# Performance work log

Hardware: AMD Instinct MI355X
Metric: run time of the kernel (lower is better)

## Reference

```python
import jax, jax.numpy as jnp
import numpy as np

N = 20000          # nodes (== virtual nodes, forced by scatter dim_size + residuals)
E = 240000         # edges
H = 256            # hidden_dim
SD = 128           # scalar_dim (mult of 0e in "128x0e+64x1o+32x2e")
FEAT = 128 + 64 * 3 + 32 * 5   # 480 = target_irreps dim
C = 4              # vn_channel


def _lin(key, din, dout):
    k1, k2 = jax.random.split(key)
    s = 1.0 / np.sqrt(din)
    w = jax.random.uniform(k1, (din, dout), jnp.float32, -s, s)
    b = jax.random.uniform(k2, (dout,), jnp.float32, -s, s)
    return w, b


def _mlp(x, w1, b1, w2, b2):
    # BaseMLP: Linear -> SiLU -> Linear (no norm, no residual, no last act)
    return jax.nn.silu(x @ w1 + b1) @ w2 + b2


def setup_inputs() -> dict:
    key = jax.random.key(0)
    ks = jax.random.split(key, 12)
    inp = {
        "node_feat": jax.random.normal(ks[0], (N, FEAT), jnp.float32),
        "node_pos": jax.random.normal(ks[1], (N, 3), jnp.float32),
        "vn_feat": jax.random.normal(ks[2], (N, H), jnp.float32),
        "vn_pos": jax.random.normal(ks[3], (N, 3 * C), jnp.float32),
        "edge_index": jax.random.randint(ks[4], (2, E), 0, N),
        "w_scalar": jax.random.normal(ks[5], (SD, SD), jnp.float32),  # e3nn o3.Linear 0e->0e path
    }
    mlps = {"cm": (SD + H + C * C, H), "vr": (H, C), "rv": (H, C * C),
            "ft": (H, H), "f2t": (H, SD), "vf": (H, H)}
    i = 6
    for name, (din, dout) in mlps.items():
        k1, k2 = jax.random.split(ks[i]); i += 1
        inp[name + "_w1"], inp[name + "_b1"] = _lin(k1, din, H)
        inp[name + "_w2"], inp[name + "_b2"] = _lin(k2, H, dout)
    return inp


def reference(node_feat, node_pos, vn_feat, vn_pos, edge_index, w_scalar,
              cm_w1, cm_b1, cm_w2, cm_b2, vr_w1, vr_b1, vr_w2, vr_b2,
              rv_w1, rv_b1, rv_w2, rv_b2, ft_w1, ft_b1, ft_w2, ft_b2,
              f2t_w1, f2t_b1, f2t_w2, f2t_b2, vf_w1, vf_b1, vf_w2, vf_b2):
    n = node_feat.shape[0]
    row, col = edge_index[0], edge_index[1]

    # e3nn o3.Linear(target_irreps -> SDx0e): single 0e->0e path, 1/sqrt(fan_in)
    nfs = (node_feat[:, :SD] @ w_scalar) * (1.0 / np.sqrt(SD))

    # per-edge relative positions between node pos (tiled to C channels) and vn pos
    d = (jnp.tile(node_pos[row], (1, C)) - vn_pos[col]).reshape(-1, C, 3)  # [E,C,3]

    # normalized gram matrix of the C difference vectors
    ip = jnp.einsum('ecj,ekj->eck', d, d).reshape(-1, C * C)
    ip = ip / jnp.maximum(jnp.linalg.norm(ip, axis=-1, keepdims=True), 1e-8)

    dn = d / jnp.maximum(jnp.linalg.norm(d, axis=-1, keepdims=True), 1e-8)  # [E,C,3]

    msg = _mlp(jnp.concatenate([nfs[row], vn_feat[col], ip], axis=1),
               cm_w1, cm_b1, cm_w2, cm_b2)                                   # [E,H]

    w_vr = _mlp(msg, vr_w1, vr_b1, vr_w2, vr_b2)                 # [E,C]
    w_rv = _mlp(msg, rv_w1, rv_b1, rv_w2, rv_b2).reshape(-1, C, C)

    inv = 1.0 / np.sqrt(C)
    # FCTP Cx1o (x) 1x0e -> 1x1o  (x2 == 1): weighted sum of the C vectors
    vr_upd = inv * jnp.einsum('ec,ecj->ej', w_vr, dn)            # [E,3]
    # FCTP Cx1o (x) 1x0e -> Cx1o on -dn
    rv_upd = inv * jnp.einsum('ecu,ecj->euj', w_rv, -dn).reshape(-1, 3 * C)  # [E,3C]

    cnt = jnp.maximum(jax.ops.segment_sum(jnp.ones((row.shape[0],), msg.dtype), row, n), 1.0)[:, None]
    agg_feat = jax.ops.segment_sum(msg, row, n) / cnt            # scatter_mean by row
    agg_vr = jax.ops.segment_sum(vr_upd, row, n) / cnt
    agg_rv = jax.ops.segment_sum(rv_upd, row, n) / cnt

    ds = _mlp(_mlp(agg_feat, ft_w1, ft_b1, ft_w2, ft_b2), f2t_w1, f2t_b1, f2t_w2, f2t_b2)
    node_feat_out = node_feat.at[:, :SD].add(ds)  # delta only hits the scalar (0e) block
    node_pos_out = node_pos + agg_vr
    vn_feat_out = vn_feat + _mlp(agg_feat, vf_w1, vf_b1, vf_w2, vf_b2)
    vn_pos_out = vn_pos + agg_rv
    return node_feat_out, node_pos_out, vn_feat_out, vn_pos_out
```

## Files before the change

kernel.cpp:

```cpp
#include <hip/hip_runtime.h>
#include <hip/hip_bf16.h>
#include <math.h>


#define FEAT 480
#define HDIM 256
#define SDIM 128
#define MSTR 264

#define OW1   0
#define OW2   106496
#define OVR1  172032
#define ORV1  237568
#define OVR2  303104
#define ORV2  307200
#define OFT1  311296
#define OFT2  376832
#define OF2T1 442368
#define OF2T2 507904
#define OVF1  540672
#define OVF2  606208
#define OWTOT 671744

typedef __attribute__((ext_vector_type(8))) short bf16x8;
typedef __attribute__((ext_vector_type(4))) float f32x4;

__device__ __forceinline__ float rcp_f(float x) {
    return __builtin_amdgcn_rcpf(x);
}
__device__ __forceinline__ float silu_f(float x) {
    return x * rcp_f(1.0f + __expf(-x));
}
__device__ __forceinline__ ushort f2b(float v) {
    __hip_bfloat16 h = __float2bfloat16(v);
    return *(ushort*)&h;
}
__device__ __forceinline__ float b2f(ushort u) {
    union { unsigned int i; float f; } c;
    c.i = ((unsigned int)u) << 16;
    return c.f;
}

#define KLOOP2(SRC, WP)                                                        \
    {                                                                          \
        _Pragma("unroll")                                                      \
        for (int mt = 0; mt < 4; ++mt)                                         \
            _Pragma("unroll")                                                  \
            for (int nt = 0; nt < 2; ++nt) acc[mt][nt] = (f32x4)0.f;           \
        _Pragma("unroll")                                                      \
        for (int ks = 0; ks < 8; ++ks) {                                       \
            bf16x8 a_[4];                                                      \
            _Pragma("unroll")                                                  \
            for (int mt = 0; mt < 4; ++mt)                                     \
                a_[mt] = *(const bf16x8*)&(SRC)[(mt * 16 + lr) * MSTR + ks * 32 + lk * 8]; \
            _Pragma("unroll")                                                  \
            for (int nt = 0; nt < 2; ++nt) {                                   \
                const bf16x8 b = *(const bf16x8*)&(WP)[(size_t)(((wv * 2 + nt) * 8 + ks) * 512) + lane * 8]; \
                _Pragma("unroll")                                              \
                for (int mt = 0; mt < 4; ++mt)                                 \
                    acc[mt][nt] = __builtin_amdgcn_mfma_f32_16x16x32_bf16(a_[mt], b, acc[mt][nt], 0, 0, 0); \
            }                                                                  \
        }                                                                      \
    }

#define EPI_SILU2(DST, BIAS)                                                   \
    _Pragma("unroll")                                                          \
    for (int nt = 0; nt < 2; ++nt) {                                           \
        const int col = colBase + nt * 16 + lr;                                \
        const float bb = (BIAS)[col];                                          \
        _Pragma("unroll")                                                      \
        for (int mt = 0; mt < 4; ++mt)                                         \
            _Pragma("unroll")                                                  \
            for (int r = 0; r < 4; ++r) {                                      \
                const int row = mt * 16 + lk * 4 + r;                          \
                (DST)[row * MSTR + col] = f2b(silu_f(acc[mt][nt][r] + bb));    \
            }                                                                  \
    }

#define KLOOP_FR(SRC, WP)                                                      \
    {                                                                          \
        _Pragma("unroll")                                                      \
        for (int mt = 0; mt < 2; ++mt)                                         \
            _Pragma("unroll")                                                  \
            for (int nt = 0; nt < 4; ++nt) accn[mt][nt] = (f32x4)0.f;          \
        _Pragma("unroll")                                                      \
        for (int ks = 0; ks < 8; ++ks) {                                       \
            const bf16x8 a0 = *(const bf16x8*)&(SRC)[lr * MSTR + ks * 32 + lk * 8];        \
            const bf16x8 a1 = *(const bf16x8*)&(SRC)[(lr + 16) * MSTR + ks * 32 + lk * 8]; \
            _Pragma("unroll")                                                  \
            for (int nt = 0; nt < 4; ++nt) {                                   \
                const bf16x8 b = *(const bf16x8*)&(WP)[(size_t)(((wv * 4 + nt) * 8 + ks) * 512) + lane * 8]; \
                accn[0][nt] = __builtin_amdgcn_mfma_f32_16x16x32_bf16(a0, b, accn[0][nt], 0, 0, 0); \
                accn[1][nt] = __builtin_amdgcn_mfma_f32_16x16x32_bf16(a1, b, accn[1][nt], 0, 0, 0); \
            }                                                                  \
        }                                                                      \
    }

#define EPI_SILUN(DST, BIAS)                                                   \
    _Pragma("unroll")                                                          \
    for (int nt = 0; nt < 4; ++nt) {                                           \
        const int col = colBase + nt * 16 + lr;                                \
        const float bb = (BIAS)[col];                                          \
        _Pragma("unroll")                                                      \
        for (int mt = 0; mt < 2; ++mt)                                         \
            _Pragma("unroll")                                                  \
            for (int r = 0; r < 4; ++r) {                                      \
                const int row = mt * 16 + lk * 4 + r;                          \
                (DST)[row * MSTR + col] = f2b(silu_f(accn[mt][nt][r] + bb));   \
            }                                                                  \
    }

__global__ __launch_bounds__(256) void k_count(
    const int* __restrict__ eidx, int* __restrict__ cnt_i, int E)
{
    const int e = blockIdx.x * 256 + threadIdx.x;
    if (e < E) atomicAdd(&cnt_i[eidx[e]], 1);
}

__global__ __launch_bounds__(1024) void k_scanA(
    const int* __restrict__ cnt_i, int* __restrict__ rowstart,
    float* __restrict__ cntf, int* __restrict__ bsum, int Nn)
{
    __shared__ int sh[1024];
    const int t = threadIdx.x;
    const int i = blockIdx.x * 1024 + t;
    const int v = (i < Nn) ? cnt_i[i] : 0;
    sh[t] = v;
    __syncthreads();
    for (int off = 1; off < 1024; off <<= 1) {
        const int add = (t >= off) ? sh[t - off] : 0;
        __syncthreads();
        sh[t] += add;
        __syncthreads();
    }
    if (i < Nn) {
        rowstart[i + 1] = sh[t];
        cntf[i] = fmaxf((float)v, 1.0f);
    }
    if (t == 1023) bsum[blockIdx.x] = sh[t];
}

__global__ __launch_bounds__(64) void k_scanB(int* __restrict__ bsum, int nb)
{
    if (threadIdx.x == 0) {
        int s = 0;
        for (int i = 0; i < nb; ++i) { const int v = bsum[i]; bsum[i] = s; s += v; }
    }
}

__global__ __launch_bounds__(1024) void k_scanC(
    int* __restrict__ rowstart, const int* __restrict__ bsum, int Nn)
{
    const int i = blockIdx.x * 1024 + threadIdx.x;
    if (i < Nn) rowstart[i + 1] += bsum[blockIdx.x];
    if (i == 0) rowstart[0] = 0;
}

__global__ __launch_bounds__(256) void k_place(
    const int* __restrict__ eidx, const int* __restrict__ rowstart,
    int* __restrict__ cursor, int* __restrict__ elist, int E)
{
    const int e = blockIdx.x * 256 + threadIdx.x;
    if (e < E) {
        const int r = eidx[e];
        const int p = atomicAdd(&cursor[r], 1);
        elist[rowstart[r] + p] = e;
    }
}

__global__ __launch_bounds__(256) void k_wprep(
    const float* __restrict__ w1, const float* __restrict__ w2,
    const float* __restrict__ vrw1, const float* __restrict__ rvw1,
    const float* __restrict__ vrw2, const float* __restrict__ rvw2,
    const float* __restrict__ ftw1, const float* __restrict__ ftw2,
    const float* __restrict__ f2tw1, const float* __restrict__ f2tw2,
    const float* __restrict__ vfw1, const float* __restrict__ vfw2,
    ushort* __restrict__ wb)
{
    const int idx = blockIdx.x * 256 + threadIdx.x;
    if (idx >= OWTOT) return;
    ushort v;
    if (idx < OW2) {
        const int o = idx, f = o >> 9, l = (o >> 3) & 63, e = o & 7;
        const int nt = f / 13, ks = f % 13;
        const int col = nt * 16 + (l & 15);
        const int k = ks * 32 + ((l >> 4) << 3) + e;
        v = (k < 400) ? f2b(w1[(size_t)k * 256 + col]) : (ushort)0;
    } else if (idx < OVR1) {
        const int o = idx - OW2, f = o >> 9, l = (o >> 3) & 63, e = o & 7;
        const int col = (f >> 3) * 16 + (l & 15);
        const int k = (f & 7) * 32 + ((l >> 4) << 3) + e;
        v = f2b(w2[(size_t)k * 256 + col]);
    } else if (idx < ORV1) {
        const int o = idx - OVR1, f = o >> 9, l = (o >> 3) & 63, e = o & 7;
        const int col = (f >> 3) * 16 + (l & 15);
        const int k = (f & 7) * 32 + ((l >> 4) << 3) + e;
        v = f2b(vrw1[(size_t)k * 256 + col]);
    } else if (idx < OVR2) {
        const int o = idx - ORV1, f = o >> 9, l = (o >> 3) & 63, e = o & 7;
        const int col = (f >> 3) * 16 + (l & 15);
        const int k = (f & 7) * 32 + ((l >> 4) << 3) + e;
        v = f2b(rvw1[(size_t)k * 256 + col]);
    } else if (idx < ORV2) {
        const int o = idx - OVR2, f = o >> 9, l = (o >> 3) & 63, e = o & 7;
        const int col = l & 15;
        const int k = f * 32 + ((l >> 4) << 3) + e;
        v = (col < 4) ? f2b(vrw2[(size_t)k * 4 + col]) : (ushort)0;
    } else if (idx < OFT1) {
        const int o = idx - ORV2, f = o >> 9, l = (o >> 3) & 63, e = o & 7;
        const int col = l & 15;
        const int k = f * 32 + ((l >> 4) << 3) + e;
        v = f2b(rvw2[(size_t)k * 16 + col]);
    } else if (idx < OFT2) {
        const int o = idx - OFT1, f = o >> 9, l = (o >> 3) & 63, e = o & 7;
        const int col = (f >> 3) * 16 + (l & 15);
        const int k = (f & 7) * 32 + ((l >> 4) << 3) + e;
        v = f2b(ftw1[(size_t)k * 256 + col]);
    } else if (idx < OF2T1) {
        const int o = idx - OFT2, f = o >> 9, l = (o >> 3) & 63, e = o & 7;
        const int col = (f >> 3) * 16 + (l & 15);
        const int k = (f & 7) * 32 + ((l >> 4) << 3) + e;
        v = f2b(ftw2[(size_t)k * 256 + col]);
    } else if (idx < OF2T2) {
        const int o = idx - OF2T1, f = o >> 9, l = (o >> 3) & 63, e = o & 7;
        const int col = (f >> 3) * 16 + (l & 15);
        const int k = (f & 7) * 32 + ((l >> 4) << 3) + e;
        v = f2b(f2tw1[(size_t)k * 256 + col]);
    } else if (idx < OVF1) {
        const int o = idx - OF2T2, f = o >> 9, l = (o >> 3) & 63, e = o & 7;
        const int col = (f >> 3) * 16 + (l & 15);
        const int k = (f & 7) * 32 + ((l >> 4) << 3) + e;
        v = f2b(f2tw2[(size_t)k * 128 + col]);
    } else if (idx < OVF2) {
        const int o = idx - OVF1, f = o >> 9, l = (o >> 3) & 63, e = o & 7;
        const int col = (f >> 3) * 16 + (l & 15);
        const int k = (f & 7) * 32 + ((l >> 4) << 3) + e;
        v = f2b(vfw1[(size_t)k * 256 + col]);
    } else {
        const int o = idx - OVF2, f = o >> 9, l = (o >> 3) & 63, e = o & 7;
        const int col = (f >> 3) * 16 + (l & 15);
        const int k = (f & 7) * 32 + ((l >> 4) << 3) + e;
        v = f2b(vfw2[(size_t)k * 256 + col]);
    }
    wb[idx] = v;
}

__global__ __launch_bounds__(256) void k_vnb(
    const float* __restrict__ vn_feat, ushort* __restrict__ vnb, int total4)
{
    const int i = blockIdx.x * 256 + threadIdx.x;
    if (i >= total4) return;
    const float4 v = *(const float4*)&vn_feat[(size_t)i * 4];
    ushort4 o;
    o.x = f2b(v.x); o.y = f2b(v.y); o.z = f2b(v.z); o.w = f2b(v.w);
    *(ushort4*)&vnb[(size_t)i * 4] = o;
}

__global__ __launch_bounds__(256) void k_nfs(
    const float* __restrict__ node_feat, const float* __restrict__ w_scalar,
    ushort* __restrict__ nfsb)
{
    __shared__ float At[32][20];
    __shared__ float Wt[16][128];
    const int t  = threadIdx.x;
    const int m0 = blockIdx.x * 32;
    const int c4 = (t & 31) * 4;
    const int rg = t >> 5;
    float acc[4][4] = {};
    for (int k0 = 0; k0 < 128; k0 += 16) {
        if (t < 128) {
            const int r = t >> 2, kk = (t & 3) * 4;
            *(float4*)&At[r][kk] =
                *(const float4*)&node_feat[(size_t)(m0 + r) * FEAT + k0 + kk];
        }
        #pragma unroll
        for (int i = 0; i < 2; ++i) {
            const int p  = t + i * 256;
            const int wr = p >> 5, wc = (p & 31) * 4;
            *(float4*)&Wt[wr][wc] =
                *(const float4*)&w_scalar[(size_t)(k0 + wr) * SDIM + wc];
        }
        __syncthreads();
        #pragma unroll
        for (int kk = 0; kk < 16; ++kk) {
            const float4 w = *(const float4*)&Wt[kk][c4];
            #pragma unroll
            for (int j = 0; j < 4; ++j) {
                const float a = At[rg * 4 + j][kk];
                acc[j][0] = fmaf(a, w.x, acc[j][0]);
                acc[j][1] = fmaf(a, w.y, acc[j][1]);
                acc[j][2] = fmaf(a, w.z, acc[j][2]);
                acc[j][3] = fmaf(a, w.w, acc[j][3]);
            }
        }
        __syncthreads();
    }
    const float s = 0.08838834764831845f;
    #pragma unroll
    for (int j = 0; j < 4; ++j) {
        ushort4 o;
        o.x = f2b(acc[j][0] * s); o.y = f2b(acc[j][1] * s);
        o.z = f2b(acc[j][2] * s); o.w = f2b(acc[j][3] * s);
        *(ushort4*)&nfsb[(size_t)(m0 + rg * 4 + j) * SDIM + c4] = o;
    }
}

__global__ __launch_bounds__(512, 4) void k_edge(
    const ushort* __restrict__ nfsb, const ushort* __restrict__ vnb,
    const float* __restrict__ node_pos, const float* __restrict__ vn_pos,
    const int* __restrict__ eidx, const int* __restrict__ elist,
    const ushort* __restrict__ wb,
    const float* __restrict__ b1, const float* __restrict__ b2,
    const float* __restrict__ vrb1, const float* __restrict__ vrb2,
    const float* __restrict__ rvb1, const float* __restrict__ rvb2,
    float* __restrict__ agg_feat, float* __restrict__ agg_vr,
    float* __restrict__ agg_rv, int E)
{
    __shared__ ushort Mg[64 * MSTR];
    __shared__ ushort Hd[64 * MSTR];
    __shared__ ushort ipB[64 * 16];
    __shared__ float dnS[64][12];
    __shared__ float wvrS[64][4];
    __shared__ float wrvS[64][16];
    __shared__ int rowi[64], coli[64];

    const int t  = threadIdx.x;
    const int e0 = blockIdx.x * 64;
    const int wv = t >> 6;
    const int lane = t & 63;
    const int lr = lane & 15;
    const int lk = lane >> 4;
    const int colBase = wv * 32;

    if (t < 64) {
        const int e = elist[e0 + t];
        const int r = eidx[e];
        const int c = eidx[E + e];
        rowi[t] = r; coli[t] = c;
        const float px = node_pos[r * 3 + 0];
        const float py = node_pos[r * 3 + 1];
        const float pz = node_pos[r * 3 + 2];
        float d[4][3];
        #pragma unroll
        for (int ch = 0; ch < 4; ++ch) {
            d[ch][0] = px - vn_pos[(size_t)c * 12 + ch * 3 + 0];
            d[ch][1] = py - vn_pos[(size_t)c * 12 + ch * 3 + 1];
            d[ch][2] = pz - vn_pos[(size_t)c * 12 + ch * 3 + 2];
        }
        float ss = 0.f, ipv[16];
        #pragma unroll
        for (int ci = 0; ci < 4; ++ci)
            #pragma unroll
            for (int ck = 0; ck < 4; ++ck) {
                const float v = d[ci][0]*d[ck][0] + d[ci][1]*d[ck][1] + d[ci][2]*d[ck][2];
                ipv[ci * 4 + ck] = v; ss += v * v;
            }
        const float inrm = rcp_f(fmaxf(sqrtf(ss), 1e-8f));
        #pragma unroll
        for (int i = 0; i < 16; ++i) ipB[t * 16 + i] = f2b(ipv[i] * inrm);
        #pragma unroll
        for (int ch = 0; ch < 4; ++ch) {
            const float nn = sqrtf(d[ch][0]*d[ch][0] + d[ch][1]*d[ch][1] + d[ch][2]*d[ch][2]);
            const float s = rcp_f(fmaxf(nn, 1e-8f));
            dnS[t][ch * 3 + 0] = d[ch][0] * s;
            dnS[t][ch * 3 + 1] = d[ch][1] * s;
            dnS[t][ch * 3 + 2] = d[ch][2] * s;
        }
    }
    __syncthreads();

    const ushort* nA[4]; const ushort* vA[4];
    #pragma unroll
    for (int mt = 0; mt < 4; ++mt) {
        nA[mt] = nfsb + (size_t)rowi[mt * 16 + lr] * SDIM + lk * 8;
        vA[mt] = vnb  + (size_t)coli[mt * 16 + lr] * HDIM + lk * 8;
    }
    const ushort* w1t = wb + OW1;

    f32x4 acc[4][2];

    #pragma unroll
    for (int mt = 0; mt < 4; ++mt)
        #pragma unroll
        for (int nt = 0; nt < 2; ++nt) acc[mt][nt] = (f32x4)0.f;
    #pragma unroll
    for (int ks = 0; ks < 13; ++ks) {
        bf16x8 a_[4];
        #pragma unroll
        for (int mt = 0; mt < 4; ++mt) {
            if (ks < 4)       a_[mt] = *(const bf16x8*)(nA[mt] + ks * 32);
            else if (ks < 12) a_[mt] = *(const bf16x8*)(vA[mt] + ks * 32 - 128);
            else if (lk < 2)  a_[mt] = *(const bf16x8*)&ipB[(mt * 16 + lr) * 16 + lk * 8];
            else              a_[mt] = (bf16x8)(short)0;
        }
        #pragma unroll
        for (int nt = 0; nt < 2; ++nt) {
            const bf16x8 b = *(const bf16x8*)&w1t[(size_t)(((wv * 2 + nt) * 13 + ks) * 512) + lane * 8];
            #pragma unroll
            for (int mt = 0; mt < 4; ++mt)
                acc[mt][nt] = __builtin_amdgcn_mfma_f32_16x16x32_bf16(a_[mt], b, acc[mt][nt], 0, 0, 0);
        }
    }
    EPI_SILU2(Hd, b1);
    __syncthreads();

    KLOOP2(Hd, wb + OW2);
    #pragma unroll
    for (int nt = 0; nt < 2; ++nt) {
        const int col = colBase + nt * 16 + lr;
        const float bb = b2[col];
        #pragma unroll
        for (int mt = 0; mt < 4; ++mt)
            #pragma unroll
            for (int r = 0; r < 4; ++r) {
                const int row = mt * 16 + lk * 4 + r;
                Mg[row * MSTR + col] = f2b(acc[mt][nt][r] + bb);
            }
    }
    __syncthreads();

    {
        const int col = t & 255;
        const int r0 = (t >> 8) * 32;
        float s = 0.f;
        int prev = rowi[r0];
        for (int r = r0; r < r0 + 32; ++r) {
            const int rr = rowi[r];
            if (rr != prev) {
                atomicAdd(&agg_feat[(size_t)prev * HDIM + col], s);
                s = 0.f; prev = rr;
            }
            s += b2f(Mg[r * MSTR + col]);
        }
        atomicAdd(&agg_feat[(size_t)prev * HDIM + col], s);
    }

    KLOOP2(Mg, wb + OVR1);
    EPI_SILU2(Hd, vrb1);

    KLOOP2(Mg, wb + ORV1);
    __syncthreads();
    #pragma unroll
    for (int nt = 0; nt < 2; ++nt) {
        const int col = colBase + nt * 16 + lr;
        const float br = rvb1[col];
        #pragma unroll
        for (int mt = 0; mt < 4; ++mt)
            #pragma unroll
            for (int r = 0; r < 4; ++r) {
                const int row = mt * 16 + lk * 4 + r;
                Mg[row * MSTR + col] = f2b(silu_f(acc[mt][nt][r] + br));
            }
    }
    __syncthreads();

    if ((wv & 3) == 0) {
        const int rb = (wv >> 2) * 32;
        const ushort* vrw2t = wb + OVR2;
        f32x4 a2[2]; a2[0] = (f32x4)0.f; a2[1] = (f32x4)0.f;
        #pragma unroll
        for (int ks = 0; ks < 8; ++ks) {
            const bf16x8 a0 = *(const bf16x8*)&Hd[(rb + lr) * MSTR + ks * 32 + lk * 8];
            const bf16x8 a1 = *(const bf16x8*)&Hd[(rb + 16 + lr) * MSTR + ks * 32 + lk * 8];
            const bf16x8 b  = *(const bf16x8*)&vrw2t[(size_t)(ks * 512) + lane * 8];
            a2[0] = __builtin_amdgcn_mfma_f32_16x16x32_bf16(a0, b, a2[0], 0, 0, 0);
            a2[1] = __builtin_amdgcn_mfma_f32_16x16x32_bf16(a1, b, a2[1], 0, 0, 0);
        }
        if (lr < 4) {
            const float bb = vrb2[lr];
            #pragma unroll
            for (int mt = 0; mt < 2; ++mt)
                #pragma unroll
                for (int r = 0; r < 4; ++r)
                    wvrS[rb + mt * 16 + lk * 4 + r][lr] = a2[mt][r] + bb;
        }
    } else if ((wv & 3) == 1) {
        const int rb = (wv >> 2) * 32;
        const ushort* rvw2t = wb + ORV2;
        f32x4 a2[2]; a2[0] = (f32x4)0.f; a2[1] = (f32x4)0.f;
        #pragma unroll
        for (int ks = 0; ks < 8; ++ks) {
            const bf16x8 a0 = *(const bf16x8*)&Mg[(rb + lr) * MSTR + ks * 32 + lk * 8];
            const bf16x8 a1 = *(const bf16x8*)&Mg[(rb + 16 + lr) * MSTR + ks * 32 + lk * 8];
            const bf16x8 b  = *(const bf16x8*)&rvw2t[(size_t)(ks * 512) + lane * 8];
            a2[0] = __builtin_amdgcn_mfma_f32_16x16x32_bf16(a0, b, a2[0], 0, 0, 0);
            a2[1] = __builtin_amdgcn_mfma_f32_16x16x32_bf16(a1, b, a2[1], 0, 0, 0);
        }
        const float bb = rvb2[lr];
        #pragma unroll
        for (int mt = 0; mt < 2; ++mt)
            #pragma unroll
            for (int r = 0; r < 4; ++r)
                wrvS[rb + mt * 16 + lk * 4 + r][lr] = a2[mt][r] + bb;
    }
    __syncthreads();

    if (t < 64) {
        float wvv[4], wrr[16], dn[12], ev[15];
        #pragma unroll
        for (int c = 0; c < 4; ++c)  wvv[c] = wvrS[t][c];
        #pragma unroll
        for (int i = 0; i < 16; ++i) wrr[i] = wrvS[t][i];
        #pragma unroll
        for (int i = 0; i < 12; ++i) dn[i]  = dnS[t][i];
        #pragma unroll
        for (int j = 0; j < 3; ++j) {
            float v = 0.f;
            #pragma unroll
            for (int c = 0; c < 4; ++c) v = fmaf(wvv[c], dn[c * 3 + j], v);
            ev[j] = 0.5f * v;
        }
        #pragma unroll
        for (int u = 0; u < 4; ++u)
            #pragma unroll
            for (int j = 0; j < 3; ++j) {
                float v = 0.f;
                #pragma unroll
                for (int c = 0; c < 4; ++c) v = fmaf(wrr[c * 4 + u], dn[c * 3 + j], v);
                ev[3 + u * 3 + j] = -0.5f * v;
            }
        #pragma unroll
        for (int i = 0; i < 15; ++i) wrvS[t][i] = ev[i];
    }
    __syncthreads();

    if ((t & 255) < 15) {
        const int comp = t & 255;
        const int r0 = (t >> 8) * 32;
        float s = 0.f;
        int prev = rowi[r0];
        for (int r = r0; r < r0 + 32; ++r) {
            const int rr = rowi[r];
            if (rr != prev) {
                if (comp < 3) atomicAdd(&agg_vr[(size_t)prev * 3 + comp], s);
                else          atomicAdd(&agg_rv[(size_t)prev * 12 + (comp - 3)], s);
                s = 0.f; prev = rr;
            }
            s += wrvS[r][comp];
        }
        if (comp < 3) atomicAdd(&agg_vr[(size_t)prev * 3 + comp], s);
        else          atomicAdd(&agg_rv[(size_t)prev * 12 + (comp - 3)], s);
    }
}

__global__ __launch_bounds__(256, 4) void k_node(
    const float* __restrict__ node_feat, const float* __restrict__ node_pos,
    const float* __restrict__ vn_feat, const float* __restrict__ vn_pos,
    const float* __restrict__ agg_feat, const float* __restrict__ agg_vr,
    const float* __restrict__ agg_rv, const float* __restrict__ cntf,
    const ushort* __restrict__ wb,
    const float* __restrict__ ftb1, const float* __restrict__ ftb2,
    const float* __restrict__ f2tb1, const float* __restrict__ f2tb2,
    const float* __restrict__ vfb1, const float* __restrict__ vfb2,
    float* __restrict__ out, int Nn)
{
    __shared__ ushort Ab[32 * MSTR];
    __shared__ ushort Hd[32 * MSTR];
    __shared__ float rc[32];
    const int t  = threadIdx.x;
    const int n0 = blockIdx.x * 32;
    const int wv = t >> 6;
    const int lane = t & 63;
    const int lr = lane & 15;
    const int lk = lane >> 4;
    const int colBase = wv * 64;

    float* nf_out = out;
    float* np_out = out + (size_t)Nn * FEAT;
    float* vf_out = np_out + (size_t)Nn * 3;
    float* vp_out = vf_out + (size_t)Nn * HDIM;

    if (t < 32) rc[t] = rcp_f(fmaxf(cntf[n0 + t], 1.0f));
    __syncthreads();
    #pragma unroll
    for (int i = 0; i < 8; ++i) {
        const int p = t + i * 256;
        const int r = p >> 6, cc = (p & 63) * 4;
        float4 v = *(const float4*)&agg_feat[(size_t)(n0 + r) * HDIM + cc];
        const float s = rc[r];
        ushort4 o;
        o.x = f2b(v.x * s); o.y = f2b(v.y * s);
        o.z = f2b(v.z * s); o.w = f2b(v.w * s);
        *(ushort4*)&Ab[r * MSTR + cc] = o;
    }
    __syncthreads();

    f32x4 accn[2][4];

    KLOOP_FR(Ab, wb + OVF1);
    EPI_SILUN(Hd, vfb1);
    __syncthreads();
    KLOOP_FR(Hd, wb + OVF2);
    #pragma unroll
    for (int nt = 0; nt < 4; ++nt) {
        const int col = colBase + nt * 16 + lr;
        const float bb = vfb2[col];
        #pragma unroll
        for (int mt = 0; mt < 2; ++mt)
            #pragma unroll
            for (int r = 0; r < 4; ++r) {
                const int row = mt * 16 + lk * 4 + r;
                const size_t o = (size_t)(n0 + row) * HDIM + col;
                vf_out[o] = vn_feat[o] + accn[mt][nt][r] + bb;
            }
    }
    __syncthreads();

    KLOOP_FR(Ab, wb + OFT1);
    EPI_SILUN(Hd, ftb1);
    __syncthreads();
    KLOOP_FR(Hd, wb + OFT2);
    #pragma unroll
    for (int nt = 0; nt < 4; ++nt) {
        const int col = colBase + nt * 16 + lr;
        const float bb = ftb2[col];
        #pragma unroll
        for (int mt = 0; mt < 2; ++mt)
            #pragma unroll
            for (int r = 0; r < 4; ++r) {
                const int row = mt * 16 + lk * 4 + r;
                Ab[row * MSTR + col] = f2b(accn[mt][nt][r] + bb);
            }
    }
    __syncthreads();

    KLOOP_FR(Ab, wb + OF2T1);
    EPI_SILUN(Hd, f2tb1);
    __syncthreads();
    {
        const ushort* w2p = wb + OF2T2;
        f32x4 a2[2][2];
        #pragma unroll
        for (int mt = 0; mt < 2; ++mt)
            #pragma unroll
            for (int nt = 0; nt < 2; ++nt) a2[mt][nt] = (f32x4)0.f;
        #pragma unroll
        for (int ks = 0; ks < 8; ++ks) {
            const int k0 = ks * 32 + lk * 8;
            const bf16x8 a0 = *(const bf16x8*)&Hd[lr * MSTR + k0];
            const bf16x8 a1 = *(const bf16x8*)&Hd[(lr + 16) * MSTR + k0];
            const bf16x8 w0 = *(const bf16x8*)&w2p[(size_t)(((wv * 2 + 0) * 8 + ks) * 512) + lane * 8];
            const bf16x8 w1v = *(const bf16x8*)&w2p[(size_t)(((wv * 2 + 1) * 8 + ks) * 512) + lane * 8];
            a2[0][0] = __builtin_amdgcn_mfma_f32_16x16x32_bf16(a0, w0, a2[0][0], 0, 0, 0);
            a2[1][0] = __builtin_amdgcn_mfma_f32_16x16x32_bf16(a1, w0, a2[1][0], 0, 0, 0);
            a2[0][1] = __builtin_amdgcn_mfma_f32_16x16x32_bf16(a0, w1v, a2[0][1], 0, 0, 0);
            a2[1][1] = __builtin_amdgcn_mfma_f32_16x16x32_bf16(a1, w1v, a2[1][1], 0, 0, 0);
        }
        #pragma unroll
        for (int nt = 0; nt < 2; ++nt) {
            const int col = wv * 32 + nt * 16 + lr;
            const float bb = f2tb2[col];
            #pragma unroll
            for (int mt = 0; mt < 2; ++mt)
                #pragma unroll
                for (int r = 0; r < 4; ++r) {
                    const int row = mt * 16 + lk * 4 + r;
                    const size_t o = (size_t)(n0 + row) * FEAT + col;
                    nf_out[o] = node_feat[o] + a2[mt][nt][r] + bb;
                }
        }
    }

    for (int p = t; p < 32 * 88; p += 256) {
        const int r = p / 88;
        const int cc = 128 + (p % 88) * 4;
        const size_t o = (size_t)(n0 + r) * FEAT + cc;
        *(float4*)&nf_out[o] = *(const float4*)&node_feat[o];
    }
    if (t < 32) {
        const int n = n0 + t;
        const float s = rc[t];
        #pragma unroll
        for (int j = 0; j < 3; ++j)
            np_out[(size_t)n * 3 + j] = node_pos[(size_t)n * 3 + j] + agg_vr[(size_t)n * 3 + j] * s;
        #pragma unroll
        for (int j = 0; j < 12; ++j)
            vp_out[(size_t)n * 12 + j] = vn_pos[(size_t)n * 12 + j] + agg_rv[(size_t)n * 12 + j] * s;
    }
}

extern "C" void kernel_launch(void* const* d_in, const int* in_sizes, int n_in,
                              void* d_out, int out_size, void* d_ws, size_t ws_size,
                              hipStream_t stream)
{
    (void)n_in; (void)out_size; (void)ws_size;
    const float* node_feat = (const float*)d_in[0];
    const float* node_pos  = (const float*)d_in[1];
    const float* vn_feat   = (const float*)d_in[2];
    const float* vn_pos    = (const float*)d_in[3];
    const int*   eidx      = (const int*)d_in[4];
    const float* w_scalar  = (const float*)d_in[5];
    const float* cm_w1  = (const float*)d_in[6];
    const float* cm_b1  = (const float*)d_in[7];
    const float* cm_w2  = (const float*)d_in[8];
    const float* cm_b2  = (const float*)d_in[9];
    const float* vr_w1  = (const float*)d_in[10];
    const float* vr_b1  = (const float*)d_in[11];
    const float* vr_w2  = (const float*)d_in[12];
    const float* vr_b2  = (const float*)d_in[13];
    const float* rv_w1  = (const float*)d_in[14];
    const float* rv_b1  = (const float*)d_in[15];
    const float* rv_w2  = (const float*)d_in[16];
    const float* rv_b2  = (const float*)d_in[17];
    const float* ft_w1  = (const float*)d_in[18];
    const float* ft_b1  = (const float*)d_in[19];
    const float* ft_w2  = (const float*)d_in[20];
    const float* ft_b2  = (const float*)d_in[21];
    const float* f2t_w1 = (const float*)d_in[22];
    const float* f2t_b1 = (const float*)d_in[23];
    const float* f2t_w2 = (const float*)d_in[24];
    const float* f2t_b2 = (const float*)d_in[25];
    const float* vf_w1  = (const float*)d_in[26];
    const float* vf_b1  = (const float*)d_in[27];
    const float* vf_w2  = (const float*)d_in[28];
    const float* vf_b2  = (const float*)d_in[29];

    const int Nn = in_sizes[0] / FEAT;
    const int E  = in_sizes[4] / 2;

    float* ws       = (float*)d_ws;
    float* agg_feat = ws;
    float* agg_vr   = agg_feat + (size_t)Nn * HDIM;
    float* agg_rv   = agg_vr   + (size_t)Nn * 3;
    float* cntf     = agg_rv   + (size_t)Nn * 12;
    int*   cnt_i    = (int*)(cntf + Nn);
    int*   cursor   = cnt_i + Nn;
    int*   rowstart = cursor + Nn;
    int*   bsum     = rowstart + Nn + 8;
    int*   elist    = bsum + 64;
    ushort* nfsb = (ushort*)(elist + E);
    ushort* vnb  = nfsb + (size_t)Nn * SDIM;
    ushort* wb   = vnb  + (size_t)Nn * HDIM;

    const size_t zero_bytes = (size_t)Nn * (HDIM + 3 + 12 + 1 + 2) * sizeof(float);
    hipMemsetAsync(agg_feat, 0, zero_bytes, stream);

    const int eg = (E + 255) / 256;
    const int sb = (Nn + 1023) / 1024;
    k_count<<<eg, 256, 0, stream>>>(eidx, cnt_i, E);
    k_scanA<<<sb, 1024, 0, stream>>>(cnt_i, rowstart, cntf, bsum, Nn);
    k_scanB<<<1, 64, 0, stream>>>(bsum, sb);
    k_scanC<<<sb, 1024, 0, stream>>>(rowstart, bsum, Nn);
    k_place<<<eg, 256, 0, stream>>>(eidx, rowstart, cursor, elist, E);
    k_wprep<<<(OWTOT + 255) / 256, 256, 0, stream>>>(
        cm_w1, cm_w2, vr_w1, rv_w1, vr_w2, rv_w2,
        ft_w1, ft_w2, f2t_w1, f2t_w2, vf_w1, vf_w2, wb);
    k_vnb<<<(Nn * 64 + 255) / 256, 256, 0, stream>>>(vn_feat, vnb, Nn * 64);
    k_nfs<<<Nn / 32, 256, 0, stream>>>(node_feat, w_scalar, nfsb);
    k_edge<<<E / 64, 512, 0, stream>>>(nfsb, vnb, node_pos, vn_pos, eidx, elist,
                                       wb, cm_b1, cm_b2, vr_b1, vr_b2, rv_b1, rv_b2,
                                       agg_feat, agg_vr, agg_rv, E);
    k_node<<<Nn / 32, 256, 0, stream>>>(node_feat, node_pos, vn_feat, vn_pos,
                                        agg_feat, agg_vr, agg_rv, cntf, wb,
                                        ft_b1, ft_b2, f2t_b1, f2t_b2, vf_b1, vf_b2,
                                        (float*)d_out, Nn);
}
```

Before: 431.8 us.

## Merge preprocessing kernels into one launch and fold block-sum scan into scanC

```diff
diff --git a/kernel.cpp b/kernel.cpp
--- a/kernel.cpp
+++ b/kernel.cpp
@@ -21,6 +21,10 @@
 #define OVF1  540672
 #define OVF2  606208
 #define OWTOT 671744
+
+#define NB_WPREP 2624
+#define NB_VNB   5000
+#define NB_NFS   625
 
 typedef __attribute__((ext_vector_type(8))) short bf16x8;
 typedef __attribute__((ext_vector_type(4))) float f32x4;
@@ -110,11 +114,141 @@
             }                                                                  \
     }
 
-__global__ __launch_bounds__(256) void k_count(
+__global__ __launch_bounds__(256) void k_prep(
+    const float* __restrict__ w1, const float* __restrict__ w2,
+    const float* __restrict__ vrw1, const float* __restrict__ rvw1,
+    const float* __restrict__ vrw2, const float* __restrict__ rvw2,
+    const float* __restrict__ ftw1, const float* __restrict__ ftw2,
+    const float* __restrict__ f2tw1, const float* __restrict__ f2tw2,
+    const float* __restrict__ vfw1, const float* __restrict__ vfw2,
+    ushort* __restrict__ wb,
+    const float* __restrict__ vn_feat, ushort* __restrict__ vnb,
+    const float* __restrict__ node_feat, const float* __restrict__ w_scalar,
+    ushort* __restrict__ nfsb,
     const int* __restrict__ eidx, int* __restrict__ cnt_i, int E)
 {
-    const int e = blockIdx.x * 256 + threadIdx.x;
-    if (e < E) atomicAdd(&cnt_i[eidx[e]], 1);
+    __shared__ float At[32][20];
+    __shared__ float Wt[16][128];
+    const int bid = blockIdx.x;
+    const int t = threadIdx.x;
+
+    if (bid < NB_WPREP) {
+        const int idx = bid * 256 + t;
+        ushort v;
+        if (idx < OW2) {
+            const int o = idx, f = o >> 9, l = (o >> 3) & 63, e = o & 7;
+            const int nt = f / 13, ks = f % 13;
+            const int col = nt * 16 + (l & 15);
+            const int k = ks * 32 + ((l >> 4) << 3) + e;
+            v = (k < 400) ? f2b(w1[(size_t)k * 256 + col]) : (ushort)0;
+        } else if (idx < OVR1) {
+            const int o = idx - OW2, f = o >> 9, l = (o >> 3) & 63, e = o & 7;
+            const int col = (f >> 3) * 16 + (l & 15);
+            const int k = (f & 7) * 32 + ((l >> 4) << 3) + e;
+            v = f2b(w2[(size_t)k * 256 + col]);
+        } else if (idx < ORV1) {
+            const int o = idx - OVR1, f = o >> 9, l = (o >> 3) & 63, e = o & 7;
+            const int col = (f >> 3) * 16 + (l & 15);
+            const int k = (f & 7) * 32 + ((l >> 4) << 3) + e;
+            v = f2b(vrw1[(size_t)k * 256 + col]);
+        } else if (idx < OVR2) {
+            const int o = idx - ORV1, f = o >> 9, l = (o >> 3) & 63, e = o & 7;
+            const int col = (f >> 3) * 16 + (l & 15);
+            const int k = (f & 7) * 32 + ((l >> 4) << 3) + e;
+            v = f2b(rvw1[(size_t)k * 256 + col]);
+        } else if (idx < ORV2) {
+            const int o = idx - OVR2, f = o >> 9, l = (o >> 3) & 63, e = o & 7;
+            const int col = l & 15;
+            const int k = f * 32 + ((l >> 4) << 3) + e;
+            v = (col < 4) ? f2b(vrw2[(size_t)k * 4 + col]) : (ushort)0;
+        } else if (idx < OFT1) {
+            const int o = idx - ORV2, f = o >> 9, l = (o >> 3) & 63, e = o & 7;
+            const int col = l & 15;
+            const int k = f * 32 + ((l >> 4) << 3) + e;
+            v = f2b(rvw2[(size_t)k * 16 + col]);
+        } else if (idx < OFT2) {
+            const int o = idx - OFT1, f = o >> 9, l = (o >> 3) & 63, e = o & 7;
+            const int col = (f >> 3) * 16 + (l & 15);
+            const int k = (f & 7) * 32 + ((l >> 4) << 3) + e;
+            v = f2b(ftw1[(size_t)k * 256 + col]);
+        } else if (idx < OF2T1) {
+            const int o = idx - OFT2, f = o >> 9, l = (o >> 3) & 63, e = o & 7;
+            const int col = (f >> 3) * 16 + (l & 15);
+            const int k = (f & 7) * 32 + ((l >> 4) << 3) + e;
+            v = f2b(ftw2[(size_t)k * 256 + col]);
+        } else if (idx < OF2T2) {
+            const int o = idx - OF2T1, f = o >> 9, l = (o >> 3) & 63, e = o & 7;
+            const int col = (f >> 3) * 16 + (l & 15);
+            const int k = (f & 7) * 32 + ((l >> 4) << 3) + e;
+            v = f2b(f2tw1[(size_t)k * 256 + col]);
+        } else if (idx < OVF1) {
+            const int o = idx - OF2T2, f = o >> 9, l = (o >> 3) & 63, e = o & 7;
+            const int col = (f >> 3) * 16 + (l & 15);
+            const int k = (f & 7) * 32 + ((l >> 4) << 3) + e;
+            v = f2b(f2tw2[(size_t)k * 128 + col]);
+        } else if (idx < OVF2) {
+            const int o = idx - OVF1, f = o >> 9, l = (o >> 3) & 63, e = o & 7;
+            const int col = (f >> 3) * 16 + (l & 15);
+            const int k = (f & 7) * 32 + ((l >> 4) << 3) + e;
+            v = f2b(vfw1[(size_t)k * 256 + col]);
+        } else {
+            const int o = idx - OVF2, f = o >> 9, l = (o >> 3) & 63, e = o & 7;
+            const int col = (f >> 3) * 16 + (l & 15);
+            const int k = (f & 7) * 32 + ((l >> 4) << 3) + e;
+            v = f2b(vfw2[(size_t)k * 256 + col]);
+        }
+        wb[idx] = v;
+    } else if (bid < NB_WPREP + NB_VNB) {
+        const int i = (bid - NB_WPREP) * 256 + t;
+        const float4 v = *(const float4*)&vn_feat[(size_t)i * 4];
+        ushort4 o;
+        o.x = f2b(v.x); o.y = f2b(v.y); o.z = f2b(v.z); o.w = f2b(v.w);
+        *(ushort4*)&vnb[(size_t)i * 4] = o;
+    } else if (bid < NB_WPREP + NB_VNB + NB_NFS) {
+        const int m0 = (bid - NB_WPREP - NB_VNB) * 32;
+        const int c4 = (t & 31) * 4;
+        const int rg = t >> 5;
+        float acc[4][4] = {};
+        for (int k0 = 0; k0 < 128; k0 += 16) {
+            if (t < 128) {
+                const int r = t >> 2, kk = (t & 3) * 4;
+                *(float4*)&At[r][kk] =
+                    *(const float4*)&node_feat[(size_t)(m0 + r) * FEAT + k0 + kk];
+            }
+            #pragma unroll
+            for (int i = 0; i < 2; ++i) {
+                const int p  = t + i * 256;
+                const int wr = p >> 5, wc = (p & 31) * 4;
+                *(float4*)&Wt[wr][wc] =
+                    *(const float4*)&w_scalar[(size_t)(k0 + wr) * SDIM + wc];
+            }
+            __syncthreads();
+            #pragma unroll
+            for (int kk = 0; kk < 16; ++kk) {
+                const float4 w = *(const float4*)&Wt[kk][c4];
+                #pragma unroll
+                for (int j = 0; j < 4; ++j) {
+                    const float a = At[rg * 4 + j][kk];
+                    acc[j][0] = fmaf(a, w.x, acc[j][0]);
+                    acc[j][1] = fmaf(a, w.y, acc[j][1]);
+                    acc[j][2] = fmaf(a, w.z, acc[j][2]);
+                    acc[j][3] = fmaf(a, w.w, acc[j][3]);
+                }
+            }
+            __syncthreads();
+        }
+        const float s = 0.08838834764831845f;
+        #pragma unroll
+        for (int j = 0; j < 4; ++j) {
+            ushort4 o;
+            o.x = f2b(acc[j][0] * s); o.y = f2b(acc[j][1] * s);
+            o.z = f2b(acc[j][2] * s); o.w = f2b(acc[j][3] * s);
+            *(ushort4*)&nfsb[(size_t)(m0 + rg * 4 + j) * SDIM + c4] = o;
+        }
+    } else {
+        const int e = (bid - NB_WPREP - NB_VNB - NB_NFS) * 256 + t;
+        if (e < E) atomicAdd(&cnt_i[eidx[e]], 1);
+    }
 }
 
 __global__ __launch_bounds__(1024) void k_scanA(
@@ -140,19 +274,19 @@
     if (t == 1023) bsum[blockIdx.x] = sh[t];
 }
 
-__global__ __launch_bounds__(64) void k_scanB(int* __restrict__ bsum, int nb)
-{
-    if (threadIdx.x == 0) {
-        int s = 0;
-        for (int i = 0; i < nb; ++i) { const int v = bsum[i]; bsum[i] = s; s += v; }
-    }
-}
-
 __global__ __launch_bounds__(1024) void k_scanC(
     int* __restrict__ rowstart, const int* __restrict__ bsum, int Nn)
 {
-    const int i = blockIdx.x * 1024 + threadIdx.x;
-    if (i < Nn) rowstart[i + 1] += bsum[blockIdx.x];
+    __shared__ int carry_s;
+    const int t = threadIdx.x;
+    if (t == 0) {
+        int s = 0;
+        for (int b = 0; b < (int)blockIdx.x; ++b) s += bsum[b];
+        carry_s = s;
+    }
+    __syncthreads();
+    const int i = blockIdx.x * 1024 + t;
+    if (i < Nn) rowstart[i + 1] += carry_s;
     if (i == 0) rowstart[0] = 0;
 }
 
@@ -165,143 +299,6 @@
         const int r = eidx[e];
         const int p = atomicAdd(&cursor[r], 1);
         elist[rowstart[r] + p] = e;
-    }
-}
-
-__global__ __launch_bounds__(256) void k_wprep(
-    const float* __restrict__ w1, const float* __restrict__ w2,
-    const float* __restrict__ vrw1, const float* __restrict__ rvw1,
-    const float* __restrict__ vrw2, const float* __restrict__ rvw2,
-    const float* __restrict__ ftw1, const float* __restrict__ ftw2,
-    const float* __restrict__ f2tw1, const float* __restrict__ f2tw2,
-    const float* __restrict__ vfw1, const float* __restrict__ vfw2,
-    ushort* __restrict__ wb)
-{
-    const int idx = blockIdx.x * 256 + threadIdx.x;
-    if (idx >= OWTOT) return;
-    ushort v;
-    if (idx < OW2) {
-        const int o = idx, f = o >> 9, l = (o >> 3) & 63, e = o & 7;
-        const int nt = f / 13, ks = f % 13;
-        const int col = nt * 16 + (l & 15);
-        const int k = ks * 32 + ((l >> 4) << 3) + e;
-        v = (k < 400) ? f2b(w1[(size_t)k * 256 + col]) : (ushort)0;
-    } else if (idx < OVR1) {
-        const int o = idx - OW2, f = o >> 9, l = (o >> 3) & 63, e = o & 7;
-        const int col = (f >> 3) * 16 + (l & 15);
-        const int k = (f & 7) * 32 + ((l >> 4) << 3) + e;
-        v = f2b(w2[(size_t)k * 256 + col]);
-    } else if (idx < ORV1) {
-        const int o = idx - OVR1, f = o >> 9, l = (o >> 3) & 63, e = o & 7;
-        const int col = (f >> 3) * 16 + (l & 15);
-        const int k = (f & 7) * 32 + ((l >> 4) << 3) + e;
-        v = f2b(vrw1[(size_t)k * 256 + col]);
-    } else if (idx < OVR2) {
-        const int o = idx - ORV1, f = o >> 9, l = (o >> 3) & 63, e = o & 7;
-        const int col = (f >> 3) * 16 + (l & 15);
-        const int k = (f & 7) * 32 + ((l >> 4) << 3) + e;
-        v = f2b(rvw1[(size_t)k * 256 + col]);
-    } else if (idx < ORV2) {
-        const int o = idx - OVR2, f = o >> 9, l = (o >> 3) & 63, e = o & 7;
-        const int col = l & 15;
-        const int k = f * 32 + ((l >> 4) << 3) + e;
-        v = (col < 4) ? f2b(vrw2[(size_t)k * 4 + col]) : (ushort)0;
-    } else if (idx < OFT1) {
-        const int o = idx - ORV2, f = o >> 9, l = (o >> 3) & 63, e = o & 7;
-        const int col = l & 15;
-        const int k = f * 32 + ((l >> 4) << 3) + e;
-        v = f2b(rvw2[(size_t)k * 16 + col]);
-    } else if (idx < OFT2) {
-        const int o = idx - OFT1, f = o >> 9, l = (o >> 3) & 63, e = o & 7;
-        const int col = (f >> 3) * 16 + (l & 15);
-        const int k = (f & 7) * 32 + ((l >> 4) << 3) + e;
-        v = f2b(ftw1[(size_t)k * 256 + col]);
-    } else if (idx < OF2T1) {
-        const int o = idx - OFT2, f = o >> 9, l = (o >> 3) & 63, e = o & 7;
-        const int col = (f >> 3) * 16 + (l & 15);
-        const int k = (f & 7) * 32 + ((l >> 4) << 3) + e;
-        v = f2b(ftw2[(size_t)k * 256 + col]);
-    } else if (idx < OF2T2) {
-        const int o = idx - OF2T1, f = o >> 9, l = (o >> 3) & 63, e = o & 7;
-        const int col = (f >> 3) * 16 + (l & 15);
-        const int k = (f & 7) * 32 + ((l >> 4) << 3) + e;
-        v = f2b(f2tw1[(size_t)k * 256 + col]);
-    } else if (idx < OVF1) {
-        const int o = idx - OF2T2, f = o >> 9, l = (o >> 3) & 63, e = o & 7;
-        const int col = (f >> 3) * 16 + (l & 15);
-        const int k = (f & 7) * 32 + ((l >> 4) << 3) + e;
-        v = f2b(f2tw2[(size_t)k * 128 + col]);
-    } else if (idx < OVF2) {
-        const int o = idx - OVF1, f = o >> 9, l = (o >> 3) & 63, e = o & 7;
-        const int col = (f >> 3) * 16 + (l & 15);
-        const int k = (f & 7) * 32 + ((l >> 4) << 3) + e;
-        v = f2b(vfw1[(size_t)k * 256 + col]);
-    } else {
-        const int o = idx - OVF2, f = o >> 9, l = (o >> 3) & 63, e = o & 7;
-        const int col = (f >> 3) * 16 + (l & 15);
-        const int k = (f & 7) * 32 + ((l >> 4) << 3) + e;
-        v = f2b(vfw2[(size_t)k * 256 + col]);
-    }
-    wb[idx] = v;
-}
-
-__global__ __launch_bounds__(256) void k_vnb(
-    const float* __restrict__ vn_feat, ushort* __restrict__ vnb, int total4)
-{
-    const int i = blockIdx.x * 256 + threadIdx.x;
-    if (i >= total4) return;
-    const float4 v = *(const float4*)&vn_feat[(size_t)i * 4];
-    ushort4 o;
-    o.x = f2b(v.x); o.y = f2b(v.y); o.z = f2b(v.z); o.w = f2b(v.w);
-    *(ushort4*)&vnb[(size_t)i * 4] = o;
-}
-
-__global__ __launch_bounds__(256) void k_nfs(
-    const float* __restrict__ node_feat, const float* __restrict__ w_scalar,
-    ushort* __restrict__ nfsb)
-{
-    __shared__ float At[32][20];
-    __shared__ float Wt[16][128];
-    const int t  = threadIdx.x;
-    const int m0 = blockIdx.x * 32;
-    const int c4 = (t & 31) * 4;
-    const int rg = t >> 5;
-    float acc[4][4] = {};
-    for (int k0 = 0; k0 < 128; k0 += 16) {
-        if (t < 128) {
-            const int r = t >> 2, kk = (t & 3) * 4;
-            *(float4*)&At[r][kk] =
-                *(const float4*)&node_feat[(size_t)(m0 + r) * FEAT + k0 + kk];
-        }
-        #pragma unroll
-        for (int i = 0; i < 2; ++i) {
-            const int p  = t + i * 256;
-            const int wr = p >> 5, wc = (p & 31) * 4;
-            *(float4*)&Wt[wr][wc] =
-                *(const float4*)&w_scalar[(size_t)(k0 + wr) * SDIM + wc];
-        }
-        __syncthreads();
-        #pragma unroll
-        for (int kk = 0; kk < 16; ++kk) {
-            const float4 w = *(const float4*)&Wt[kk][c4];
-            #pragma unroll
-            for (int j = 0; j < 4; ++j) {
-                const float a = At[rg * 4 + j][kk];
-                acc[j][0] = fmaf(a, w.x, acc[j][0]);
-                acc[j][1] = fmaf(a, w.y, acc[j][1]);
-                acc[j][2] = fmaf(a, w.z, acc[j][2]);
-                acc[j][3] = fmaf(a, w.w, acc[j][3]);
-            }
-        }
-        __syncthreads();
-    }
-    const float s = 0.08838834764831845f;
-    #pragma unroll
-    for (int j = 0; j < 4; ++j) {
-        ushort4 o;
-        o.x = f2b(acc[j][0] * s); o.y = f2b(acc[j][1] * s);
-        o.z = f2b(acc[j][2] * s); o.w = f2b(acc[j][3] * s);
-        *(ushort4*)&nfsb[(size_t)(m0 + rg * 4 + j) * SDIM + c4] = o;
     }
 }
 
@@ -737,16 +734,14 @@
 
     const int eg = (E + 255) / 256;
     const int sb = (Nn + 1023) / 1024;
-    k_count<<<eg, 256, 0, stream>>>(eidx, cnt_i, E);
+    k_prep<<<NB_WPREP + NB_VNB + NB_NFS + eg, 256, 0, stream>>>(
+        cm_w1, cm_w2, vr_w1, rv_w1, vr_w2, rv_w2,
+        ft_w1, ft_w2, f2t_w1, f2t_w2, vf_w1, vf_w2, wb,
+        vn_feat, vnb, node_feat, w_scalar, nfsb,
+        eidx, cnt_i, E);
     k_scanA<<<sb, 1024, 0, stream>>>(cnt_i, rowstart, cntf, bsum, Nn);
-    k_scanB<<<1, 64, 0, stream>>>(bsum, sb);
     k_scanC<<<sb, 1024, 0, stream>>>(rowstart, bsum, Nn);
     k_place<<<eg, 256, 0, stream>>>(eidx, rowstart, cursor, elist, E);
-    k_wprep<<<(OWTOT + 255) / 256, 256, 0, stream>>>(
-        cm_w1, cm_w2, vr_w1, rv_w1, vr_w2, rv_w2,
-        ft_w1, ft_w2, f2t_w1, f2t_w2, vf_w1, vf_w2, wb);
-    k_vnb<<<(Nn * 64 + 255) / 256, 256, 0, stream>>>(vn_feat, vnb, Nn * 64);
-    k_nfs<<<Nn / 32, 256, 0, stream>>>(node_feat, w_scalar, nfsb);
     k_edge<<<E / 64, 512, 0, stream>>>(nfsb, vnb, node_pos, vn_pos, eidx, elist,
                                        wb, cm_b1, cm_b2, vr_b1, vr_b2, rv_b1, rv_b2,
                                        agg_feat, agg_vr, agg_rv, E);
```

Result: faster. 423.4 us (-2.0%).
